# Kernel optimization log

Hardware: AMD Instinct MI355X
Metric: run time of the kernel (lower is better)

Reference implementation:

```python
import jax, jax.numpy as jnp
import numpy as np
from jax import lax

SHIFT_SIZE = 5
PAD = SHIFT_SIZE // 2


def _chunk_shifts(C):
    # torch.chunk(x, 5, dim=1): chunk size = ceil(C/5); shift for chunk i is i - PAD
    csz = -(-C // SHIFT_SIZE)
    return jnp.arange(C) // csz - PAD  # (C,) in [-PAD, PAD]


def _shift_along_h(x, shifts):
    # x: (B,C,H,W). Equivalent of pad+chunk+roll(dim=2)+cat+narrow: per-channel
    # zero-filled shift along H (no wraparound since |shift| <= PAD).
    B, C, H, W = x.shape
    xp = jnp.pad(x, ((0, 0), (0, 0), (PAD, PAD), (0, 0)))
    c_idx = jnp.arange(C)[:, None]              # (C,1)
    h_idx = jnp.arange(H)[None, :] + PAD - shifts[:, None]  # (C,H)
    return xp[:, c_idx, h_idx, :]               # (B,C,H,W)


def _shift_along_w(x, shifts):
    return jnp.swapaxes(_shift_along_h(jnp.swapaxes(x, 2, 3), shifts), 2, 3)


def setup_inputs() -> dict:
    key = jax.random.key(0)
    ks = jax.random.split(key, 7)
    B, H, W, C, hidden = 8, 128, 128, 256, 256
    x = jax.random.normal(ks[0], (B, H * W, C), dtype=jnp.float32)
    w1 = jax.random.normal(ks[1], (hidden, C), dtype=jnp.float32) * 0.02
    b1 = jnp.zeros((hidden,), dtype=jnp.float32)
    fan_out = 3 * 3 * hidden // hidden  # groups = hidden
    dw_w = jax.random.normal(ks[2], (hidden, 1, 3, 3), dtype=jnp.float32) * np.sqrt(2.0 / fan_out)
    dw_b = jnp.zeros((hidden,), dtype=jnp.float32)
    w2 = jax.random.normal(ks[3], (C, hidden), dtype=jnp.float32) * 0.02
    b2 = jnp.zeros((C,), dtype=jnp.float32)
    return {"x": x, "H": H, "W": W, "w1": w1, "b1": b1,
            "dw_w": dw_w, "dw_b": dw_b, "w2": w2, "b2": b2}


def reference(x, H, W, w1, b1, dw_w, dw_b, w2, b2):
    B, N, C = x.shape
    shifts = _chunk_shifts(C)

    # --- shift along H, then fc1 ---
    xn = jnp.reshape(jnp.swapaxes(x, 1, 2), (B, C, H, W))
    x_s = _shift_along_h(xn, shifts)
    x_s = jnp.swapaxes(x_s.reshape(B, C, H * W), 1, 2)   # (B,N,C)
    h = x_s @ w1.T + b1                                  # (B,N,hidden)

    # --- depthwise 3x3 conv ---
    Ch = h.shape[-1]
    himg = jnp.reshape(jnp.swapaxes(h, 1, 2), (B, Ch, H, W))
    himg = lax.conv_general_dilated(
        himg, dw_w, window_strides=(1, 1), padding=((1, 1), (1, 1)),
        feature_group_count=Ch,
        dimension_numbers=("NCHW", "OIHW", "NCHW")) + dw_b[None, :, None, None]
    h = jnp.swapaxes(himg.reshape(B, Ch, H * W), 1, 2)

    h = jax.nn.gelu(h, approximate=False)

    # --- shift along W, then fc2 ---
    hn = jnp.reshape(jnp.swapaxes(h, 1, 2), (B, Ch, H, W))
    h_s = _shift_along_w(hn, _chunk_shifts(Ch))
    h_s = jnp.swapaxes(h_s.reshape(B, Ch, H * W), 1, 2)  # (B,N,hidden)
    out = h_s @ w2.T + b2                                # (B,N,C)
    return out
```

## Files before the change

kernel.cpp:

```cpp
#include <hip/hip_runtime.h>
#include <hip/hip_bf16.h>
#include <math.h>

#define Hc   128
#define Wc   128
#define Cc   256
#define Nc   (Hc * Wc)
#define Bn   8
#define Mtot (Bn * Nc)
#define CSZ  52
#define SPAD 2

typedef unsigned short ushort4v __attribute__((ext_vector_type(4)));
typedef unsigned short ushort8  __attribute__((ext_vector_type(8)));
typedef __bf16         bf16x8   __attribute__((ext_vector_type(8)));
typedef float          f32x4    __attribute__((ext_vector_type(4)));

__device__ __forceinline__ float bf2f(unsigned short u) {
    return __uint_as_float(((unsigned)u) << 16);
}
__device__ __forceinline__ unsigned short f2bf(float f) {
    unsigned u = __float_as_uint(f);
    return (unsigned short)((u + 0x7fffu + ((u >> 16) & 1u)) >> 16);
}
__device__ __forceinline__ unsigned pk2bf(float a, float b) {
    unsigned ua = __float_as_uint(a) + 0x8000u;
    unsigned ub = __float_as_uint(b) + 0x8000u;
    return __builtin_amdgcn_perm(ub, ua, 0x07060302);
}
__device__ __forceinline__ void async16(const void* g, void* l) {
    __builtin_amdgcn_global_load_lds(
        (const __attribute__((address_space(1))) unsigned*)g,
        (__attribute__((address_space(3))) unsigned*)l, 16, 0, 0);
}

__global__ __launch_bounds__(256)
void wprep_kernel(const float* __restrict__ w1, const float* __restrict__ w2,
                  const float* __restrict__ dw_w,
                  unsigned short* __restrict__ w1b, unsigned short* __restrict__ w2b,
                  float* __restrict__ dwT)
{
    const int g = blockIdx.x * 256 + threadIdx.x;
    {
        float4 a = *(const float4*)(w1 + (size_t)g * 4);
        ushort4v o = { f2bf(a.x), f2bf(a.y), f2bf(a.z), f2bf(a.w) };
        *(ushort4v*)(w1b + (size_t)g * 4) = o;
    }
    {
        float4 a = *(const float4*)(w2 + (size_t)g * 4);
        ushort4v o = { f2bf(a.x), f2bf(a.y), f2bf(a.z), f2bf(a.w) };
        *(ushort4v*)(w2b + (size_t)g * 4) = o;
    }
    if (g < 9 * Cc) dwT[(g % 9) * Cc + g / 9] = dw_w[g];
}

__global__ __launch_bounds__(256)
void shiftcvt_kernel(const float* __restrict__ x, unsigned short* __restrict__ xb)
{
    const int gid0 = blockIdx.x * 256 + threadIdx.x;
#pragma unroll
    for (int it = 0; it < 4; ++it) {
        const int gid = gid0 + it * (4096 * 256);
        const int row = gid >> 5;
        const int c   = (gid & 31) * 8;
        const int hh  = (row >> 7) & 127;
        const int s0  = c / CSZ - SPAD;
        const int s1  = (c + 4) / CSZ - SPAD;
        const int h0  = hh - s0, h1r = hh - s1;
        float4 v0 = make_float4(0.f, 0.f, 0.f, 0.f);
        float4 v1 = make_float4(0.f, 0.f, 0.f, 0.f);
        if (h0  >= 0 && h0  < Hc)
            v0 = *(const float4*)(x + ((size_t)row + (size_t)(h0 - hh) * Wc) * Cc + c);
        if (h1r >= 0 && h1r < Hc)
            v1 = *(const float4*)(x + ((size_t)row + (size_t)(h1r - hh) * Wc) * Cc + c + 4);
        uint4 o;
        o.x = pk2bf(v0.x, v0.y); o.y = pk2bf(v0.z, v0.w);
        o.z = pk2bf(v1.x, v1.y); o.w = pk2bf(v1.z, v1.w);
        *(uint4*)(xb + (size_t)row * Cc + c) = o;
    }
}

__global__ __launch_bounds__(256)
void fc1_mfma_kernel(const unsigned short* __restrict__ xb, const unsigned short* __restrict__ w1b,
                     const float* __restrict__ b1, unsigned short* __restrict__ h1)
{
    __shared__ __align__(16) unsigned char smem[34816];
    __bf16* As = (__bf16*)smem;
    __bf16* Bs = (__bf16*)(smem + 16384);
    unsigned short* Cs = (unsigned short*)smem;

    const int tid  = threadIdx.x;
    const int lane = tid & 63;
    const int wave = tid >> 6;
    const int wm = (wave >> 1) * 64, wn = (wave & 1) * 64;

    const int lid = ((blockIdx.x & 7) << 8) | (blockIdx.x >> 3);
    const int bx  = lid >> 1;
    const int j0  = (lid & 1) * 128;
    const size_t m0 = (size_t)bx * 128;
    const int idx0 = tid, idx1 = tid + 256;

    const size_t aro0 = (m0 + (idx0 >> 2)) * Cc + (idx0 & 3) * 8;
    const size_t aro1 = (m0 + (idx1 >> 2)) * Cc + (idx1 & 3) * 8;
    const size_t bro0 = (size_t)(j0 + (idx0 >> 2)) * Cc + (idx0 & 3) * 8;
    const size_t bro1 = (size_t)(j0 + (idx1 >> 2)) * Cc + (idx1 & 3) * 8;

    auto stage = [&](int buf, int t) {
        const int k0 = t * 32;
        __bf16* adst = As + buf * 4096;
        __bf16* bdst = Bs + buf * 4096;
        async16(xb  + aro0 + k0, adst + idx0 * 8);
        async16(xb  + aro1 + k0, adst + idx1 * 8);
        async16(w1b + bro0 + k0, bdst + idx0 * 8);
        async16(w1b + bro1 + k0, bdst + idx1 * 8);
    };

    f32x4 acc[4][4] = {};
    const int kq = (lane >> 4) * 8;
    const int rr = lane & 15;

    stage(0, 0);
    __syncthreads();

    int cur = 0;
    for (int t = 0; t < 8; ++t) {
        const int nxt = cur ^ 1;
        if (t < 7) stage(nxt, t + 1);
        bf16x8 a[4], b[4];
        const __bf16* ap = As + cur * 4096;
        const __bf16* bp = Bs + cur * 4096;
#pragma unroll
        for (int i = 0; i < 4; ++i) {
            a[i] = *(const bf16x8*)(ap + (wm + i * 16 + rr) * 32 + kq);
            b[i] = *(const bf16x8*)(bp + (wn + i * 16 + rr) * 32 + kq);
        }
#pragma unroll
        for (int i = 0; i < 4; ++i)
#pragma unroll
            for (int j = 0; j < 4; ++j)
                acc[i][j] = __builtin_amdgcn_mfma_f32_16x16x32_bf16(a[i], b[j], acc[i][j], 0, 0, 0);
        __syncthreads();
        cur = nxt;
    }

    const int cq = (lane >> 4) * 4;
    const int cc = lane & 15;
    float bv[4];
#pragma unroll
    for (int j = 0; j < 4; ++j) bv[j] = b1[j0 + wn + j * 16 + cc];
#pragma unroll
    for (int i = 0; i < 4; ++i)
#pragma unroll
        for (int j = 0; j < 4; ++j) {
            const int col = wn + j * 16 + cc;
#pragma unroll
            for (int rg = 0; rg < 4; ++rg)
                Cs[(wm + i * 16 + cq + rg) * 136 + col] = f2bf(acc[i][j][rg] + bv[j]);
        }
    __syncthreads();
    {
        const int row = tid >> 1, hf = tid & 1;
        const unsigned short* src = Cs + row * 136 + hf * 64;
        unsigned short* dst = h1 + (m0 + row) * Cc + j0 + hf * 64;
#pragma unroll
        for (int i = 0; i < 8; ++i)
            *(uint4*)(dst + i * 8) = *(const uint4*)(src + i * 8);
    }
}

__global__ __launch_bounds__(256)
void dwfc2_kernel(const unsigned short* __restrict__ h1,
                  const float* __restrict__ dwT, const float* __restrict__ dw_b,
                  const unsigned short* __restrict__ w2b, const float* __restrict__ b2,
                  float* __restrict__ out)
{
    __shared__ __align__(16) unsigned char smem[81920];
    unsigned char* Ash = smem;
    __bf16* Bs = (__bf16*)(smem + 65536);

    const int tid  = threadIdx.x;
    const int lane = tid & 63;
    const int wave = tid >> 6;

    const int lid = ((blockIdx.x & 7) << 7) | (blockIdx.x >> 3);
    const int bb = lid >> 7, hh = lid & 127;
    const size_t m0 = (size_t)lid * 128;

    {
        uint4 z; z.x = z.y = z.z = z.w = 0u;
        unsigned char* p = Ash + tid * 256;
#pragma unroll
        for (int i = 0; i < 16; ++i) *(uint4*)(p + i * 16) = z;
    }
    __syncthreads();

    {
        const int cg = tid & 31;
        const int wq = tid >> 5;
        const int c0 = cg * 8;
        const int s0 = c0 / CSZ - SPAD;
        const int s1 = (c0 + 4) / CSZ - SPAD;

        float bias[8];
        {
            float4 a0 = *(const float4*)(dw_b + c0);
            float4 a1 = *(const float4*)(dw_b + c0 + 4);
            bias[0] = a0.x; bias[1] = a0.y; bias[2] = a0.z; bias[3] = a0.w;
            bias[4] = a1.x; bias[5] = a1.y; bias[6] = a1.z; bias[7] = a1.w;
        }
        float wt[3][3][8];
#pragma unroll
        for (int dy = 0; dy < 3; ++dy)
#pragma unroll
            for (int tx = 0; tx < 3; ++tx) {
                const float* wp = dwT + (dy * 3 + tx) * Cc + c0;
                float4 wa = *(const float4*)(wp);
                float4 wb = *(const float4*)(wp + 4);
                wt[dy][tx][0] = wa.x; wt[dy][tx][1] = wa.y;
                wt[dy][tx][2] = wa.z; wt[dy][tx][3] = wa.w;
                wt[dy][tx][4] = wb.x; wt[dy][tx][5] = wb.y;
                wt[dy][tx][6] = wb.z; wt[dy][tx][7] = wb.w;
            }

#pragma unroll 1
        for (int qtr = 0; qtr < 4; ++qtr) {
            const int wbase = qtr * 32 + wq * 4 - 1;
            float acc[4][8];
#pragma unroll
            for (int i = 0; i < 4; ++i)
#pragma unroll
                for (int c = 0; c < 8; ++c) acc[i][c] = bias[c];

#pragma unroll
            for (int dy = -1; dy <= 1; ++dy) {
                const int y = hh + dy;
                if (y < 0 || y >= Hc) continue;
                const unsigned short* rp = h1 + ((size_t)bb * Nc + (size_t)y * Wc) * Cc + c0;
                float in[6][8];
#pragma unroll
                for (int dx = 0; dx < 6; ++dx) {
                    const int w = wbase + dx;
                    ushort8 raw = {0, 0, 0, 0, 0, 0, 0, 0};
                    if (w >= 0 && w < Wc) raw = *(const ushort8*)(rp + (size_t)w * Cc);
#pragma unroll
                    for (int c = 0; c < 8; ++c) in[dx][c] = bf2f(raw[c]);
                }
#pragma unroll
                for (int i = 0; i < 4; ++i)
#pragma unroll
                    for (int tx = 0; tx < 3; ++tx)
#pragma unroll
                        for (int c = 0; c < 8; ++c)
                            acc[i][c] += in[i + tx][c] * wt[dy + 1][tx][c];
            }

#pragma unroll
            for (int i = 0; i < 4; ++i) {
                float g[8];
#pragma unroll
                for (int c = 0; c < 8; ++c) {
                    const float v = acc[i][c];
                    const float u = v * v;
                    const float a = __builtin_fmaf(0.0713548162f, u, 1.5957691216f);
                    const float e = __expf(v * a);
                    g[c] = v * e * __builtin_amdgcn_rcpf(e + 1.0f);
                }
                uint2 lo, hi;
                lo.x = pk2bf(g[0], g[1]); lo.y = pk2bf(g[2], g[3]);
                hi.x = pk2bf(g[4], g[5]); hi.y = pk2bf(g[6], g[7]);
                const int wo = wbase + 1 + i;
                const int w0 = wo + s0, w1 = wo + s1;
                if ((unsigned)w0 < (unsigned)Wc)
                    *(uint2*)(Ash + w0 * 512 + ((c0 * 2) ^ ((w0 & 7) << 4))) = lo;
                if ((unsigned)w1 < (unsigned)Wc)
                    *(uint2*)(Ash + w1 * 512 + (((c0 + 4) * 2) ^ ((w1 & 7) << 4))) = hi;
            }
        }
    }

    const int wm = (wave >> 1) * 64, wn = (wave & 1) * 64;
    const int kq = (lane >> 4) * 8;
    const int rr = lane & 15;
    const int xof = (rr & 7) << 4;
    const int idx0 = tid, idx1 = tid + 256;
    const int cq = (lane >> 4) * 4;
    const int cc = lane & 15;

#pragma unroll 1
    for (int pass = 0; pass < 2; ++pass) {
        const int j0 = pass * 128;
        const size_t bro0 = (size_t)(j0 + (idx0 >> 2)) * Cc + (idx0 & 3) * 8;
        const size_t bro1 = (size_t)(j0 + (idx1 >> 2)) * Cc + (idx1 & 3) * 8;

        auto stageB = [&](int buf, int t) {
            const int k0 = t * 32;
            __bf16* bdst = Bs + buf * 4096;
            async16(w2b + bro0 + k0, bdst + idx0 * 8);
            async16(w2b + bro1 + k0, bdst + idx1 * 8);
        };

        f32x4 acc[4][4] = {};
        stageB(0, 0);
        __syncthreads();

        int cur = 0;
        for (int t = 0; t < 8; ++t) {
            const int nxt = cur ^ 1;
            if (t < 7) stageB(nxt, t + 1);
            const int k0 = t * 32;
            bf16x8 a[4], b[4];
            const __bf16* bp = Bs + cur * 4096;
#pragma unroll
            for (int i = 0; i < 4; ++i) {
                a[i] = *(const bf16x8*)(Ash + (wm + i * 16 + rr) * 512 + (((k0 + kq) * 2) ^ xof));
                b[i] = *(const bf16x8*)(bp + (wn + i * 16 + rr) * 32 + kq);
            }
#pragma unroll
            for (int i = 0; i < 4; ++i)
#pragma unroll
                for (int j = 0; j < 4; ++j)
                    acc[i][j] = __builtin_amdgcn_mfma_f32_16x16x32_bf16(a[i], b[j], acc[i][j], 0, 0, 0);
            __syncthreads();
            cur = nxt;
        }

        float bv[4];
#pragma unroll
        for (int j = 0; j < 4; ++j) bv[j] = b2[j0 + wn + j * 16 + cc];
#pragma unroll
        for (int i = 0; i < 4; ++i)
#pragma unroll
            for (int j = 0; j < 4; ++j) {
                const int col = j0 + wn + j * 16 + cc;
#pragma unroll
                for (int rg = 0; rg < 4; ++rg)
                    out[(m0 + wm + i * 16 + cq + rg) * Cc + col] = acc[i][j][rg] + bv[j];
            }
    }
}

extern "C" void kernel_launch(void* const* d_in, const int* in_sizes, int n_in,
                              void* d_out, int out_size, void* d_ws, size_t ws_size,
                              hipStream_t stream) {
    const float* x    = (const float*)d_in[0];
    const float* w1   = (const float*)d_in[3];
    const float* b1   = (const float*)d_in[4];
    const float* dw_w = (const float*)d_in[5];
    const float* dw_b = (const float*)d_in[6];
    const float* w2   = (const float*)d_in[7];
    const float* b2   = (const float*)d_in[8];
    float* out = (float*)d_out;

    unsigned short* h1  = (unsigned short*)d_ws;
    unsigned short* xb  = h1 + (size_t)Mtot * Cc;
    unsigned short* w1b = xb + (size_t)Mtot * Cc;
    unsigned short* w2b = w1b + 65536;
    float*          dwT = (float*)(w2b + 65536);

    wprep_kernel<<<dim3(64), dim3(256), 0, stream>>>(w1, w2, dw_w, w1b, w2b, dwT);
    shiftcvt_kernel<<<dim3(4096), dim3(256), 0, stream>>>(x, xb);
    fc1_mfma_kernel<<<dim3(2 * Mtot / 128), dim3(256), 0, stream>>>(xb, w1b, b1, h1);
    dwfc2_kernel<<<dim3(Mtot / 128), dim3(256), 0, stream>>>(h1, dwT, dw_b, w2b, b2, out);
}
```

Before: 363.2 us.

## Pipeline depthwise conv per K-slice with fc2 MFMA and split output columns across blocks

```diff
diff --git a/kernel.cpp b/kernel.cpp
--- a/kernel.cpp
+++ b/kernel.cpp
@@ -174,169 +174,154 @@
                   const unsigned short* __restrict__ w2b, const float* __restrict__ b2,
                   float* __restrict__ out)
 {
-    __shared__ __align__(16) unsigned char smem[81920];
-    unsigned char* Ash = smem;
-    __bf16* Bs = (__bf16*)(smem + 65536);
+    __shared__ __align__(16) unsigned char smem[32768];
+    __bf16* Ash = (__bf16*)smem;
+    __bf16* Bs  = (__bf16*)(smem + 16384);
 
     const int tid  = threadIdx.x;
     const int lane = tid & 63;
     const int wave = tid >> 6;
-
-    const int lid = ((blockIdx.x & 7) << 7) | (blockIdx.x >> 3);
-    const int bb = lid >> 7, hh = lid & 127;
-    const size_t m0 = (size_t)lid * 128;
-
-    {
-        uint4 z; z.x = z.y = z.z = z.w = 0u;
-        unsigned char* p = Ash + tid * 256;
-#pragma unroll
-        for (int i = 0; i < 16; ++i) *(uint4*)(p + i * 16) = z;
-    }
-    __syncthreads();
-
-    {
-        const int cg = tid & 31;
-        const int wq = tid >> 5;
-        const int c0 = cg * 8;
-        const int s0 = c0 / CSZ - SPAD;
-        const int s1 = (c0 + 4) / CSZ - SPAD;
-
-        float bias[8];
-        {
-            float4 a0 = *(const float4*)(dw_b + c0);
-            float4 a1 = *(const float4*)(dw_b + c0 + 4);
-            bias[0] = a0.x; bias[1] = a0.y; bias[2] = a0.z; bias[3] = a0.w;
-            bias[4] = a1.x; bias[5] = a1.y; bias[6] = a1.z; bias[7] = a1.w;
-        }
-        float wt[3][3][8];
-#pragma unroll
-        for (int dy = 0; dy < 3; ++dy)
+    const int wm = (wave >> 1) * 64, wn = (wave & 1) * 64;
+
+    const int lid = ((blockIdx.x & 7) << 8) | (blockIdx.x >> 3);
+    const int bx  = lid >> 1;
+    const int j0  = (lid & 1) * 128;
+    const int bb  = bx >> 7, hh = bx & 127;
+    const size_t m0 = (size_t)bx * 128;
+
+    const int tc = tid & 7, tw = tid >> 3;
+
+    const int idx0 = tid, idx1 = tid + 256;
+    const size_t bro0 = (size_t)(j0 + (idx0 >> 2)) * Cc + (idx0 & 3) * 8;
+    const size_t bro1 = (size_t)(j0 + (idx1 >> 2)) * Cc + (idx1 & 3) * 8;
+    auto stageB = [&](int buf, int t) {
+        const int k0 = t * 32;
+        __bf16* bdst = Bs + buf * 4096;
+        async16(w2b + bro0 + k0, bdst + idx0 * 8);
+        async16(w2b + bro1 + k0, bdst + idx1 * 8);
+    };
+
+    uint2 inr[3][6];
+    auto loadsDW = [&](int t) {
+        const int c0g = t * 32 + tc * 4;
+        const int s   = c0g / CSZ - SPAD;
+        const int wp  = tw * 4 - s;
+#pragma unroll
+        for (int dy = 0; dy < 3; ++dy) {
+            const int y = hh + dy - 1;
+            const bool oky = (unsigned)y < (unsigned)Hc;
+            const unsigned short* rp = h1 + ((size_t)bb * Nc + (size_t)y * Wc) * Cc + c0g;
+#pragma unroll
+            for (int dx = 0; dx < 6; ++dx) {
+                const int wi = wp - 1 + dx;
+                uint2 v; v.x = 0u; v.y = 0u;
+                if (oky && (unsigned)wi < (unsigned)Wc)
+                    v = *(const uint2*)(rp + (size_t)wi * Cc);
+                inr[dy][dx] = v;
+            }
+        }
+    };
+    auto mathDW = [&](int t, int buf) {
+        const int c0g = t * 32 + tc * 4;
+        const int s   = c0g / CSZ - SPAD;
+        const int wp  = tw * 4 - s;
+        float4 bv = *(const float4*)(dw_b + c0g);
+        float acc4[4][4];
+#pragma unroll
+        for (int i = 0; i < 4; ++i) {
+            acc4[i][0] = bv.x; acc4[i][1] = bv.y; acc4[i][2] = bv.z; acc4[i][3] = bv.w;
+        }
+#pragma unroll
+        for (int dy = 0; dy < 3; ++dy) {
+            float fin[6][4];
+#pragma unroll
+            for (int dx = 0; dx < 6; ++dx) {
+                const uint2 r = inr[dy][dx];
+                fin[dx][0] = bf2f((unsigned short)(r.x & 0xffffu));
+                fin[dx][1] = bf2f((unsigned short)(r.x >> 16));
+                fin[dx][2] = bf2f((unsigned short)(r.y & 0xffffu));
+                fin[dx][3] = bf2f((unsigned short)(r.y >> 16));
+            }
 #pragma unroll
             for (int tx = 0; tx < 3; ++tx) {
-                const float* wp = dwT + (dy * 3 + tx) * Cc + c0;
-                float4 wa = *(const float4*)(wp);
-                float4 wb = *(const float4*)(wp + 4);
-                wt[dy][tx][0] = wa.x; wt[dy][tx][1] = wa.y;
-                wt[dy][tx][2] = wa.z; wt[dy][tx][3] = wa.w;
-                wt[dy][tx][4] = wb.x; wt[dy][tx][5] = wb.y;
-                wt[dy][tx][6] = wb.z; wt[dy][tx][7] = wb.w;
+                const float4 wv = *(const float4*)(dwT + (dy * 3 + tx) * Cc + c0g);
+#pragma unroll
+                for (int i = 0; i < 4; ++i) {
+                    acc4[i][0] = __builtin_fmaf(fin[i + tx][0], wv.x, acc4[i][0]);
+                    acc4[i][1] = __builtin_fmaf(fin[i + tx][1], wv.y, acc4[i][1]);
+                    acc4[i][2] = __builtin_fmaf(fin[i + tx][2], wv.z, acc4[i][2]);
+                    acc4[i][3] = __builtin_fmaf(fin[i + tx][3], wv.w, acc4[i][3]);
+                }
             }
-
-#pragma unroll 1
-        for (int qtr = 0; qtr < 4; ++qtr) {
-            const int wbase = qtr * 32 + wq * 4 - 1;
-            float acc[4][8];
-#pragma unroll
-            for (int i = 0; i < 4; ++i)
-#pragma unroll
-                for (int c = 0; c < 8; ++c) acc[i][c] = bias[c];
-
-#pragma unroll
-            for (int dy = -1; dy <= 1; ++dy) {
-                const int y = hh + dy;
-                if (y < 0 || y >= Hc) continue;
-                const unsigned short* rp = h1 + ((size_t)bb * Nc + (size_t)y * Wc) * Cc + c0;
-                float in[6][8];
-#pragma unroll
-                for (int dx = 0; dx < 6; ++dx) {
-                    const int w = wbase + dx;
-                    ushort8 raw = {0, 0, 0, 0, 0, 0, 0, 0};
-                    if (w >= 0 && w < Wc) raw = *(const ushort8*)(rp + (size_t)w * Cc);
-#pragma unroll
-                    for (int c = 0; c < 8; ++c) in[dx][c] = bf2f(raw[c]);
-                }
-#pragma unroll
-                for (int i = 0; i < 4; ++i)
-#pragma unroll
-                    for (int tx = 0; tx < 3; ++tx)
-#pragma unroll
-                        for (int c = 0; c < 8; ++c)
-                            acc[i][c] += in[i + tx][c] * wt[dy + 1][tx][c];
+        }
+#pragma unroll
+        for (int i = 0; i < 4; ++i) {
+            const bool valid = (unsigned)(wp + i) < (unsigned)Wc;
+            float g[4];
+#pragma unroll
+            for (int c = 0; c < 4; ++c) {
+                const float v = acc4[i][c];
+                const float u = v * v;
+                const float a = __builtin_fmaf(0.0713548162f, u, 1.5957691216f);
+                const float e = __expf(v * a);
+                g[c] = valid ? (v * e * __builtin_amdgcn_rcpf(e + 1.0f)) : 0.f;
             }
-
-#pragma unroll
-            for (int i = 0; i < 4; ++i) {
-                float g[8];
-#pragma unroll
-                for (int c = 0; c < 8; ++c) {
-                    const float v = acc[i][c];
-                    const float u = v * v;
-                    const float a = __builtin_fmaf(0.0713548162f, u, 1.5957691216f);
-                    const float e = __expf(v * a);
-                    g[c] = v * e * __builtin_amdgcn_rcpf(e + 1.0f);
-                }
-                uint2 lo, hi;
-                lo.x = pk2bf(g[0], g[1]); lo.y = pk2bf(g[2], g[3]);
-                hi.x = pk2bf(g[4], g[5]); hi.y = pk2bf(g[6], g[7]);
-                const int wo = wbase + 1 + i;
-                const int w0 = wo + s0, w1 = wo + s1;
-                if ((unsigned)w0 < (unsigned)Wc)
-                    *(uint2*)(Ash + w0 * 512 + ((c0 * 2) ^ ((w0 & 7) << 4))) = lo;
-                if ((unsigned)w1 < (unsigned)Wc)
-                    *(uint2*)(Ash + w1 * 512 + (((c0 + 4) * 2) ^ ((w1 & 7) << 4))) = hi;
-            }
-        }
-    }
-
-    const int wm = (wave >> 1) * 64, wn = (wave & 1) * 64;
+            uint2 o; o.x = pk2bf(g[0], g[1]); o.y = pk2bf(g[2], g[3]);
+            const int row  = tw * 4 + i;
+            const int eoff = (tc * 4) ^ (((row >> 2) & 3) << 3);
+            *(uint2*)(Ash + buf * 4096 + row * 32 + eoff) = o;
+        }
+    };
+
+    f32x4 acc[4][4] = {};
     const int kq = (lane >> 4) * 8;
     const int rr = lane & 15;
-    const int xof = (rr & 7) << 4;
-    const int idx0 = tid, idx1 = tid + 256;
+
+    loadsDW(0);
+    stageB(0, 0);
+    mathDW(0, 0);
+    __syncthreads();
+
+    int cur = 0;
+    for (int t = 0; t < 8; ++t) {
+        const int nxt = cur ^ 1;
+        if (t < 7) {
+            stageB(nxt, t + 1);
+            loadsDW(t + 1);
+        }
+        bf16x8 a[4], b[4];
+        const __bf16* ap = Ash + cur * 4096;
+        const __bf16* bp = Bs  + cur * 4096;
+#pragma unroll
+        for (int i = 0; i < 4; ++i) {
+            const int rowA = wm + i * 16 + rr;
+            a[i] = *(const bf16x8*)(ap + rowA * 32 + (kq ^ (((rowA >> 2) & 3) << 3)));
+            b[i] = *(const bf16x8*)(bp + (wn + i * 16 + rr) * 32 + kq);
+        }
+#pragma unroll
+        for (int i = 0; i < 4; ++i)
+#pragma unroll
+            for (int j = 0; j < 4; ++j)
+                acc[i][j] = __builtin_amdgcn_mfma_f32_16x16x32_bf16(a[i], b[j], acc[i][j], 0, 0, 0);
+        if (t < 7) mathDW(t + 1, nxt);
+        __syncthreads();
+        cur = nxt;
+    }
+
     const int cq = (lane >> 4) * 4;
     const int cc = lane & 15;
-
-#pragma unroll 1
-    for (int pass = 0; pass < 2; ++pass) {
-        const int j0 = pass * 128;
-        const size_t bro0 = (size_t)(j0 + (idx0 >> 2)) * Cc + (idx0 & 3) * 8;
-        const size_t bro1 = (size_t)(j0 + (idx1 >> 2)) * Cc + (idx1 & 3) * 8;
-
-        auto stageB = [&](int buf, int t) {
-            const int k0 = t * 32;
-            __bf16* bdst = Bs + buf * 4096;
-            async16(w2b + bro0 + k0, bdst + idx0 * 8);
-            async16(w2b + bro1 + k0, bdst + idx1 * 8);
-        };
-
-        f32x4 acc[4][4] = {};
-        stageB(0, 0);
-        __syncthreads();
-
-        int cur = 0;
-        for (int t = 0; t < 8; ++t) {
-            const int nxt = cur ^ 1;
-            if (t < 7) stageB(nxt, t + 1);
-            const int k0 = t * 32;
-            bf16x8 a[4], b[4];
-            const __bf16* bp = Bs + cur * 4096;
-#pragma unroll
-            for (int i = 0; i < 4; ++i) {
-                a[i] = *(const bf16x8*)(Ash + (wm + i * 16 + rr) * 512 + (((k0 + kq) * 2) ^ xof));
-                b[i] = *(const bf16x8*)(bp + (wn + i * 16 + rr) * 32 + kq);
-            }
-#pragma unroll
-            for (int i = 0; i < 4; ++i)
-#pragma unroll
-                for (int j = 0; j < 4; ++j)
-                    acc[i][j] = __builtin_amdgcn_mfma_f32_16x16x32_bf16(a[i], b[j], acc[i][j], 0, 0, 0);
-            __syncthreads();
-            cur = nxt;
-        }
-
-        float bv[4];
-#pragma unroll
-        for (int j = 0; j < 4; ++j) bv[j] = b2[j0 + wn + j * 16 + cc];
-#pragma unroll
-        for (int i = 0; i < 4; ++i)
-#pragma unroll
-            for (int j = 0; j < 4; ++j) {
-                const int col = j0 + wn + j * 16 + cc;
-#pragma unroll
-                for (int rg = 0; rg < 4; ++rg)
-                    out[(m0 + wm + i * 16 + cq + rg) * Cc + col] = acc[i][j][rg] + bv[j];
-            }
-    }
+    float bv[4];
+#pragma unroll
+    for (int j = 0; j < 4; ++j) bv[j] = b2[j0 + wn + j * 16 + cc];
+#pragma unroll
+    for (int i = 0; i < 4; ++i)
+#pragma unroll
+        for (int j = 0; j < 4; ++j) {
+            const int col = j0 + wn + j * 16 + cc;
+#pragma unroll
+            for (int rg = 0; rg < 4; ++rg)
+                out[(m0 + wm + i * 16 + cq + rg) * Cc + col] = acc[i][j][rg] + bv[j];
+        }
 }
 
 extern "C" void kernel_launch(void* const* d_in, const int* in_sizes, int n_in,
@@ -360,5 +345,5 @@
     wprep_kernel<<<dim3(64), dim3(256), 0, stream>>>(w1, w2, dw_w, w1b, w2b, dwT);
     shiftcvt_kernel<<<dim3(4096), dim3(256), 0, stream>>>(x, xb);
     fc1_mfma_kernel<<<dim3(2 * Mtot / 128), dim3(256), 0, stream>>>(xb, w1b, b1, h1);
-    dwfc2_kernel<<<dim3(Mtot / 128), dim3(256), 0, stream>>>(h1, dwT, dw_b, w2b, b2, out);
-}
+    dwfc2_kernel<<<dim3(2 * Mtot / 128), dim3(256), 0, stream>>>(h1, dwT, dw_b, w2b, b2, out);
+}
```

Result: slower. 392.1 us (+8.0%).
